# Kernel tuning notes

Hardware: AMD Instinct MI355X
Metric: run time of the kernel (lower is better)

Reference implementation:

```python
import jax, jax.numpy as jnp
import numpy as np

B, N, C = 8, 4096, 768
H, HD = 12, 64          # num_heads, head_dim = C // H
M = HD * 2              # rand_feat_dim
LAM = 0.3
NUM_STEP = 5


def setup_inputs() -> dict:
    key = jax.random.key(0)
    k1, k2, k3, k4 = jax.random.split(key, 4)
    x = jax.random.normal(k1, (B, N, C), dtype=jnp.float32)
    Wqkv = jax.random.normal(k2, (C, 2 * C), dtype=jnp.float32) * 0.02
    Wproj = jax.random.normal(k3, (C, C), dtype=jnp.float32) * 0.02
    bproj = jnp.zeros((C,), dtype=jnp.float32)
    rand_matrix = jax.random.normal(k4, (H, HD, M), dtype=jnp.float32)
    return {"x": x, "Wqkv": Wqkv, "Wproj": Wproj, "bproj": bproj,
            "rand_matrix": rand_matrix}


def _soft(z, t):
    # sign(z) * relu(|z| - t): soft-thresholding (ISTA proximal step)
    return jnp.sign(z) * jax.nn.relu(jnp.abs(z) - t)


def reference(x, Wqkv, Wproj, bproj, rand_matrix):
    Bn, Nn, Cn = x.shape
    Hh, hd, m = rand_matrix.shape
    scale = hd ** (-0.5)

    qkv = x @ Wqkv                                   # [B,N,2C]
    q = qkv[..., :Cn].reshape(Bn, Nn, Hh, hd).transpose(0, 2, 1, 3)  # [B,H,N,hd]
    v = qkv[..., Cn:].reshape(Bn, Nn, Hh, hd).transpose(0, 2, 1, 3)  # [B,H,N,hd]

    # random-feature map: exp(q @ proj - ||q||^2 / 2) / sqrt(m)
    qs = q * scale ** 0.5
    rf = jnp.exp(jnp.einsum('bhnd,hdm->bhnm', qs, rand_matrix)
                 - 0.5 * jnp.sum(qs * qs, axis=-1, keepdims=True)) / m ** 0.5
    # F.normalize(p=2, dim=-2): normalize over the sequence axis
    qn = rf / jnp.maximum(jnp.linalg.norm(rf, axis=-2, keepdims=True), 1e-12)

    kk = jnp.einsum('bhnm,bhnp->bhmp', qn, qn)       # [B,H,m,m]
    kv = jnp.einsum('bhnm,bhnd->bhmd', qn, v)        # [B,H,m,hd]

    # Lipschitz bound: max row L1 norm of kk, detached
    L = jax.lax.stop_gradient(
        jnp.max(jnp.sum(jnp.abs(kk), axis=-1), axis=-1))[..., None, None] + 1.0

    # unrolled ISTA soft-thresholding loop
    s = _soft(kv, LAM)
    for _ in range(NUM_STEP):
        s = _soft(s - (kk @ s - kv) / L, LAM / L)

    out = jnp.einsum('bhnm,bhmd->bhnd', qn, s)       # [B,H,N,hd]
    out = out.transpose(0, 2, 1, 3).reshape(Bn, Nn, Cn)
    return out @ Wproj + bproj
```

## Files before the change

kernel.cpp:

```cpp
#include <hip/hip_runtime.h>


typedef __attribute__((ext_vector_type(8))) short bf16x8;
typedef __attribute__((ext_vector_type(4))) float f32x4;

#define GLD16(gptr, lptr)                                                              \
  __builtin_amdgcn_global_load_lds((const __attribute__((address_space(1))) void*)(gptr), \
                                   (__attribute__((address_space(3))) void*)(lptr), 16, 0, 0)

__device__ __forceinline__ unsigned short f2bf(float f) {
  union { float f; unsigned int u; } v; v.f = f;
  unsigned int r = v.u + 0x7fffu + ((v.u >> 16) & 1u);
  return (unsigned short)(r >> 16);
}
__device__ __forceinline__ float bf2f(unsigned short s) {
  union { unsigned int u; float f; } v; v.u = ((unsigned int)s) << 16;
  return v.f;
}
__device__ __forceinline__ float rn_of(float css) {
  return 1.f / fmaxf(sqrtf(css), 1e-12f);
}

template<int NT>
__device__ __forceinline__ void gemm256_core(
    const unsigned short* __restrict__ A,
    const unsigned short* __restrict__ B,
    int ldk,
    f32x4 (&acc)[8][4],
    unsigned short* smem) {
  const int tid = threadIdx.x;
  const int lane = tid & 63, wave = tid >> 6;
  const int l16 = lane & 15, quad = lane >> 4;
  const int wr = wave >> 2, wc = wave & 3;
  const int rsw = l16 & 7;

#pragma unroll
  for (int i = 0; i < 8; i++)
#pragma unroll
    for (int j = 0; j < 4; j++)
#pragma unroll
      for (int r = 0; r < 4; r++) acc[i][j][r] = 0.f;

  const int srow0 = tid >> 3, sc0 = ((tid & 7) ^ (srow0 & 7)) << 3;
  const int srow1 = (tid + 512) >> 3, sc1 = ((tid & 7) ^ (srow1 & 7)) << 3;
  const int dstw = wave * 512;

  auto stage = [&](int T) {
    unsigned short* d0 = smem + (T & 1) * 32768;
#pragma unroll
    for (int h = 0; h < 2; h++) {
      const unsigned short* gA = A + (long)(h * 128) * ldk + T * 64;
      const unsigned short* gB = B + (long)(h * 128) * ldk + T * 64;
      GLD16(gA + (long)srow0 * ldk + sc0, d0 + h * 8192 + dstw);
      GLD16(gA + (long)srow1 * ldk + sc1, d0 + h * 8192 + 4096 + dstw);
      GLD16(gB + (long)srow0 * ldk + sc0, d0 + 16384 + h * 8192 + dstw);
      GLD16(gB + (long)srow1 * ldk + sc1, d0 + 16384 + h * 8192 + 4096 + dstw);
    }
  };

  bf16x8 afA[4], afB[4], bnA[4], bnB[4];

  auto rdA = [&](bf16x8 (&d)[4], int b, int mh, int ks) {
    const unsigned short* p = smem + b * 32768 + wr * 8192 + (mh * 64 + l16) * 64;
#pragma unroll
    for (int ii = 0; ii < 4; ii++)
      d[ii] = *(const bf16x8*)(p + ii * 1024 + (((ks * 4 + quad) ^ rsw) << 3));
  };
  auto rdB = [&](bf16x8 (&d)[4], int b, int ks) {
    const unsigned short* p = smem + b * 32768 + 16384 + (wc >> 1) * 8192 +
                              ((wc & 1) * 64 + l16) * 64;
#pragma unroll
    for (int jj = 0; jj < 4; jj++)
      d[jj] = *(const bf16x8*)(p + jj * 1024 + (((ks * 4 + quad) ^ rsw) << 3));
  };

  auto mma = [&](int mh, bf16x8 (&a)[4], bf16x8 (&bn)[4]) {
    __builtin_amdgcn_s_setprio(1);
#pragma unroll
    for (int ii = 0; ii < 4; ii++)
#pragma unroll
      for (int jj = 0; jj < 4; jj++)
        acc[mh * 4 + ii][jj] = __builtin_amdgcn_mfma_f32_16x16x32_bf16(
            a[ii], bn[jj], acc[mh * 4 + ii][jj], 0, 0, 0);
    __builtin_amdgcn_s_setprio(0);
  };

#define FENCE asm volatile("" ::: "memory")
#define SGB __builtin_amdgcn_sched_barrier(0)
#define LGKM(n) asm volatile("s_waitcnt lgkmcnt(" #n ")" ::: "memory")
#define VMC0 asm volatile("s_waitcnt vmcnt(0)" ::: "memory")

  stage(0); stage(1);
  asm volatile("s_waitcnt vmcnt(8)" ::: "memory");
  __builtin_amdgcn_s_barrier();
  rdA(afA, 0, 0, 0); rdB(bnA, 0, 0);
  FENCE;

#pragma unroll 1
  for (int t = 0; t < NT; t++) {
    const int b = t & 1;
    const bool last = (t == NT - 1);
    rdA(afB, b, 1, 0);
    LGKM(4); SGB;
    mma(0, afA, bnA);
    rdA(afA, b, 0, 1); rdB(bnB, b, 1);
    LGKM(8); SGB;
    mma(1, afB, bnA);
    VMC0; FENCE;
    __builtin_amdgcn_s_barrier();
    FENCE;
    rdA(afB, b, 1, 1);
    LGKM(4); SGB;
    mma(0, afA, bnB);
    if (!last) { rdA(afA, b ^ 1, 0, 0); rdB(bnA, b ^ 1, 0); LGKM(8); }
    else       { LGKM(0); }
    SGB;
    mma(1, afB, bnB);
    FENCE;
    __builtin_amdgcn_s_barrier();
    FENCE;
    if (t + 2 < NT) stage(t + 2);
  }
#undef FENCE
#undef SGB
#undef LGKM
#undef VMC0
}

__global__ __launch_bounds__(256) void k_convert_bf16(const float* __restrict__ in,
                                                      unsigned short* __restrict__ out, long n4) {
  long i = (long)blockIdx.x * 256 + threadIdx.x;
  if (i < n4) {
    float4 v = ((const float4*)in)[i];
    unsigned short o[4] = {f2bf(v.x), f2bf(v.y), f2bf(v.z), f2bf(v.w)};
    ((uint2*)out)[i] = *(uint2*)o;
  }
}

__global__ __launch_bounds__(256) void k_transpose_tiled(const float* __restrict__ in,
                                                         unsigned short* __restrict__ out,
                                                         int R, int C, float scale) {
  __shared__ float t[32][33];
  const float* ib = in + (long)blockIdx.z * R * C;
  unsigned short* ob = out + (long)blockIdx.z * R * C;
  int c0 = blockIdx.x * 32, r0 = blockIdx.y * 32;
  int tx = threadIdx.x & 31, ty = threadIdx.x >> 5;
#pragma unroll
  for (int k = 0; k < 32; k += 8)
    t[ty + k][tx] = ib[(long)(r0 + ty + k) * C + c0 + tx];
  __syncthreads();
#pragma unroll
  for (int k = 0; k < 32; k += 8)
    ob[(long)(c0 + ty + k) * R + r0 + tx] = f2bf(t[tx][ty + k] * scale);
}

__global__ __launch_bounds__(512, 2) void k_gemm_qkv256(const unsigned short* __restrict__ xbf,
                                                        const unsigned short* __restrict__ wqkvT,
                                                        unsigned short* __restrict__ q,
                                                        unsigned short* __restrict__ vT) {
  __shared__ __align__(16) unsigned short smem[65536];
  f32x4 acc[8][4];
  const int L = blockIdx.x;
  const int xcd = L & 7, slot = L >> 3;
  const int rt = xcd * 16 + slot / 6;
  const int ct = slot % 6;
  gemm256_core<12>(xbf + (long)rt * 256 * 768, wqkvT + (long)ct * 256 * 768, 768, acc, smem);

  const int tid = threadIdx.x, lane = tid & 63, wave = tid >> 6;
  const int l16 = lane & 15, quad = lane >> 4;
  const int wr = wave >> 2, wc = wave & 3;
  const int b = rt >> 4;
  const int nbase = (rt & 15) * 256;
  if (ct < 3) {
#pragma unroll
    for (int i = 0; i < 8; i++)
#pragma unroll
      for (int j = 0; j < 4; j++) {
        int col = ct * 256 + wc * 64 + j * 16 + l16;
        int h = col >> 6, d = col & 63;
#pragma unroll
        for (int r = 0; r < 4; r++) {
          int n = nbase + wr * 128 + i * 16 + quad * 4 + r;
          q[((long)(b * 12 + h) * 4096 + n) * 64 + d] = f2bf(acc[i][j][r]);
        }
      }
  } else {
    unsigned short* pool = smem;
    for (int hh = 0; hh < 2; hh++) {
      __syncthreads();
      if (wr == hh) {
#pragma unroll
        for (int i = 0; i < 8; i++)
#pragma unroll
          for (int j = 0; j < 4; j++)
#pragma unroll
            for (int r = 0; r < 4; r++)
              pool[(wc * 64 + j * 16 + l16) * 136 + i * 16 + quad * 4 + r] = f2bf(acc[i][j][r]);
      }
      __syncthreads();
#pragma unroll
      for (int it = 0; it < 8; it++) {
        int chunk = it * 512 + tid;
        int col = chunk >> 4, ng = chunk & 15;
        uint4 val = *(const uint4*)&pool[col * 136 + ng * 8];
        int vcol = (ct - 3) * 256 + col;
        int h = vcol >> 6, d = vcol & 63;
        long n = nbase + hh * 128 + ng * 8;
        *(uint4*)&vT[((long)(b * 12 + h) * 64 + d) * 4096 + n] = val;
      }
    }
  }
}

__global__ __launch_bounds__(256) void k_gemm_rf(const unsigned short* __restrict__ q,
                                                 const unsigned short* __restrict__ rmT,
                                                 unsigned short* __restrict__ qnT,
                                                 float* __restrict__ colss) {
  __shared__ __align__(16) unsigned short smem[16384];
  __shared__ float hnp[256];
  __shared__ float css[128];
  unsigned short* Asm = smem;
  unsigned short* Bsm = smem + 8192;
  unsigned short* pool = smem;
  f32x4 acc[4][4];
  const int nt = blockIdx.x, bh = blockIdx.y, h = bh % 12;
  const int tid = threadIdx.x, lane = tid & 63, wave = tid >> 6;
  const int l16 = lane & 15, quad = lane >> 4;
  const int wm = (wave >> 1) * 64, wn = (wave & 1) * 64;
  const int fsw = (l16 >> 1) & 3;
  const unsigned short* Aq = q + ((long)bh * 4096 + nt * 128) * 64;
  const unsigned short* Brm = rmT + (long)h * 8192;

#pragma unroll
  for (int c = 0; c < 4; c++) {
    int chunk = c * 256 + tid;
    int row = chunk >> 3, ko8 = chunk & 7;
    int kc = ko8 >> 2;
    int c2s = (ko8 & 3) ^ ((row >> 1) & 3);
    *(uint4*)(Asm + kc * 4096 + row * 32 + c2s * 8) = *(const uint4*)(Aq + (long)row * 64 + ko8 * 8);
    *(uint4*)(Bsm + kc * 4096 + row * 32 + c2s * 8) = *(const uint4*)(Brm + (long)row * 64 + ko8 * 8);
  }
  for (int i = tid; i < 128; i += 256) css[i] = 0.f;
  __syncthreads();
  {
    const unsigned short* ap = Asm + (tid & 1) * 4096 + (tid >> 1) * 32;
    float ssum = 0.f;
#pragma unroll
    for (int e = 0; e < 32; e++) { float f = bf2f(ap[e]); ssum += f * f; }
    hnp[tid] = ssum;
  }
#pragma unroll
  for (int i = 0; i < 4; i++)
#pragma unroll
    for (int j = 0; j < 4; j++)
#pragma unroll
      for (int r = 0; r < 4; r++) acc[i][j][r] = 0.f;
#pragma unroll
  for (int kc = 0; kc < 2; kc++) {
    bf16x8 af[4], bfr[4];
#pragma unroll
    for (int i = 0; i < 4; i++)
      af[i] = *(const bf16x8*)(Asm + kc * 4096 + (wm + i * 16 + l16) * 32 + ((quad ^ fsw) * 8));
#pragma unroll
    for (int j = 0; j < 4; j++)
      bfr[j] = *(const bf16x8*)(Bsm + kc * 4096 + (wn + j * 16 + l16) * 32 + ((quad ^ fsw) * 8));
#pragma unroll
    for (int i = 0; i < 4; i++)
#pragma unroll
      for (int j = 0; j < 4; j++)
        acc[i][j] = __builtin_amdgcn_mfma_f32_16x16x32_bf16(af[i], bfr[j], acc[i][j], 0, 0, 0);
  }
  __syncthreads();
  float hnv[4][4];
#pragma unroll
  for (int i = 0; i < 4; i++)
#pragma unroll
    for (int r = 0; r < 4; r++) {
      int row = wm + i * 16 + quad * 4 + r;
      hnv[i][r] = 0.0625f * (hnp[2 * row] + hnp[2 * row + 1]);
    }
#pragma unroll
  for (int j = 0; j < 4; j++) {
    int col = wn + j * 16 + l16;
    float cp = 0.f;
#pragma unroll
    for (int i = 0; i < 4; i++)
#pragma unroll
      for (int r = 0; r < 4; r++) {
        float v = __expf(acc[i][j][r] - hnv[i][r]) * 0.08838834764831845f;
        acc[i][j][r] = v;
        cp += v * v;
      }
    atomicAdd(&css[col], cp);
  }
  __syncthreads();
  for (int i = tid; i < 128; i += 256) atomicAdd(&colss[bh * 128 + i], css[i]);
  for (int hh = 0; hh < 2; hh++) {
    __syncthreads();
    if ((wave >> 1) == hh) {
#pragma unroll
      for (int i = 0; i < 4; i++)
#pragma unroll
        for (int j = 0; j < 4; j++)
#pragma unroll
          for (int r = 0; r < 4; r++)
            pool[(i * 16 + quad * 4 + r) * 134 + wn + j * 16 + l16] = f2bf(acc[i][j][r]);
    }
    __syncthreads();
#pragma unroll
    for (int c = 0; c < 4; c++) {
      int chunk = tid + c * 256;
      int m = chunk >> 3, nj = (chunk & 7) * 8;
      unsigned short o[8];
#pragma unroll
      for (int e = 0; e < 8; e++) o[e] = pool[(nj + e) * 134 + m];
      *(uint4*)&qnT[((long)bh * 128 + m) * 4096 + nt * 128 + hh * 64 + nj] = *(uint4*)o;
    }
  }
}

__global__ __launch_bounds__(256) void k_gemm_kkkv(const unsigned short* __restrict__ qnT,
                                                   const unsigned short* __restrict__ vT,
                                                   const float* __restrict__ colss,
                                                   unsigned short* __restrict__ kkp) {
  __shared__ __align__(16) unsigned short As[128 * 32], Bs[64 * 32];
  f32x4 acc[4][6];
  const int ks = blockIdx.x, bh = blockIdx.y;
  const unsigned short* A = qnT + (long)bh * 128 * 4096 + ks * 512;
  const unsigned short* B1 = vT + (long)bh * 64 * 4096 + ks * 512;
  const int tid = threadIdx.x, lane = tid & 63, wave = tid >> 6;
  const int l16 = lane & 15, quad = lane >> 4;
  const int wm = (wave >> 1) * 64, wn = (wave & 1) * 96;
  const int arow = tid >> 2;
  const int akos = (((tid & 3) ^ ((arow >> 1) & 3)) << 3);
  const int fsw = (l16 >> 1) & 3;
#pragma unroll
  for (int i = 0; i < 4; i++)
#pragma unroll
    for (int j = 0; j < 6; j++)
#pragma unroll
      for (int r = 0; r < 4; r++) acc[i][j][r] = 0.f;
  for (int k0 = 0; k0 < 512; k0 += 32) {
    __syncthreads();
    GLD16(A + (long)arow * 4096 + k0 + akos, As + wave * 512);
    GLD16(A + (long)(arow + 64) * 4096 + k0 + akos, As + 2048 + wave * 512);
    GLD16(B1 + (long)arow * 4096 + k0 + akos, Bs + wave * 512);
    __syncthreads();
    bf16x8 af[4], bfr[6];
#pragma unroll
    for (int i = 0; i < 4; i++)
      af[i] = *(const bf16x8*)(As + (wm + i * 16 + l16) * 32 + ((quad ^ fsw) * 8));
#pragma unroll
    for (int j = 0; j < 6; j++) {
      int row = wn + j * 16 + l16;
      const unsigned short* rp = (row < 128) ? (As + row * 32) : (Bs + (row - 128) * 32);
      bfr[j] = *(const bf16x8*)(rp + ((quad ^ fsw) * 8));
    }
#pragma unroll
    for (int i = 0; i < 4; i++)
#pragma unroll
      for (int j = 0; j < 6; j++)
        acc[i][j] = __builtin_amdgcn_mfma_f32_16x16x32_bf16(af[i], bfr[j], acc[i][j], 0, 0, 0);
  }
  unsigned short* dst = kkp + ((long)ks * 96 + bh) * 24576;
  float rnr[4][4];
#pragma unroll
  for (int i = 0; i < 4; i++)
#pragma unroll
    for (int r = 0; r < 4; r++)
      rnr[i][r] = rn_of(colss[bh * 128 + wm + i * 16 + quad * 4 + r]);
#pragma unroll
  for (int j = 0; j < 6; j++) {
    int col = wn + j * 16 + l16;
    float rnc = (col < 128) ? rn_of(colss[bh * 128 + col]) : 1.f;
#pragma unroll
    for (int i = 0; i < 4; i++)
#pragma unroll
      for (int r = 0; r < 4; r++) {
        int row = wm + i * 16 + quad * 4 + r;
        dst[row * 192 + col] = f2bf(acc[i][j][r] * rnr[i][r] * rnc);
      }
  }
}

__global__ __launch_bounds__(256) void k_ista(const unsigned short* __restrict__ kkp,
                                              const float* __restrict__ colss,
                                              unsigned short* __restrict__ sT) {
  __shared__ __align__(16) unsigned short kks[128 * 144];
  __shared__ __align__(16) unsigned short ssT[64 * 144];
  __shared__ float kvs[128 * 64];
  __shared__ float red[128];
  __shared__ float rns[128];
  const int tid = threadIdx.x, lane = tid & 63, wave = tid >> 6;
  const int l16 = lane & 15, quad = lane >> 4;
  const int wm = (wave >> 1) * 64, wn = (wave & 1) * 32;
  const int bh = blockIdx.x;
  const unsigned short* base = kkp + (long)bh * 24576;
  for (int idx = tid; idx < 3072; idx += 256) {
    int m = idx / 24, c8 = idx % 24;
    float f[8] = {0.f, 0.f, 0.f, 0.f, 0.f, 0.f, 0.f, 0.f};
#pragma unroll
    for (int ks = 0; ks < 8; ks++) {
      union { uint4 u; unsigned short s[8]; } u;
      u.u = *(const uint4*)(base + (long)ks * 2359296 + m * 192 + c8 * 8);
#pragma unroll
      for (int e = 0; e < 8; e++) f[e] += bf2f(u.s[e]);
    }
    if (c8 < 16) {
#pragma unroll
      for (int e = 0; e < 8; e++) kks[m * 144 + c8 * 8 + e] = f2bf(f[e]);
    } else {
#pragma unroll
      for (int e = 0; e < 8; e++) kvs[m * 64 + (c8 - 16) * 8 + e] = f[e];
    }
  }
  __syncthreads();
  float kv[4][2][4];
#pragma unroll
  for (int i = 0; i < 4; i++)
#pragma unroll
    for (int j = 0; j < 2; j++)
#pragma unroll
      for (int r = 0; r < 4; r++) {
        int m = wm + i * 16 + quad * 4 + r, d = wn + j * 16 + l16;
        kv[i][j][r] = kvs[m * 64 + d];
      }
  if (tid < 128) {
    float rs = 0.f;
    const unsigned short* rp = kks + tid * 144;
    for (int p = 0; p < 128; p++) rs += fabsf(bf2f(rp[p]));
    red[tid] = rs;
    rns[tid] = rn_of(colss[bh * 128 + tid]);
  }
  __syncthreads();
  for (int o = 64; o > 0; o >>= 1) {
    if (tid < o) red[tid] = fmaxf(red[tid], red[tid + o]);
    __syncthreads();
  }
  const float L = red[0] + 1.f;
  const float invL = 1.f / L;
  const float lamL = 0.3f * invL;
  float sreg[4][2][4];
#pragma unroll
  for (int i = 0; i < 4; i++)
#pragma unroll
    for (int j = 0; j < 2; j++)
#pragma unroll
      for (int r = 0; r < 4; r++) {
        float z = kv[i][j][r];
        float az = fabsf(z) - 0.3f;
        float s = az > 0.f ? copysignf(az, z) : 0.f;
        sreg[i][j][r] = s;
        ssT[(wn + j * 16 + l16) * 144 + wm + i * 16 + quad * 4 + r] = f2bf(s);
      }
  for (int step = 0; step < 5; step++) {
    __syncthreads();
    f32x4 acc[4][2];
#pragma unroll
    for (int i = 0; i < 4; i++)
#pragma unroll
      for (int j = 0; j < 2; j++)
#pragma unroll
        for (int r = 0; r < 4; r++) acc[i][j][r] = 0.f;
#pragma unroll
    for (int kc = 0; kc < 4; kc++) {
      bf16x8 af[4], bfj[2];
#pragma unroll
      for (int i = 0; i < 4; i++)
        af[i] = *(const bf16x8*)(kks + (wm + i * 16 + l16) * 144 + kc * 32 + quad * 8);
#pragma unroll
      for (int j = 0; j < 2; j++)
        bfj[j] = *(const bf16x8*)(ssT + (wn + j * 16 + l16) * 144 + kc * 32 + quad * 8);
#pragma unroll
      for (int i = 0; i < 4; i++)
#pragma unroll
        for (int j = 0; j < 2; j++)
          acc[i][j] = __builtin_amdgcn_mfma_f32_16x16x32_bf16(af[i], bfj[j], acc[i][j], 0, 0, 0);
    }
    __syncthreads();
#pragma unroll
    for (int i = 0; i < 4; i++)
#pragma unroll
      for (int j = 0; j < 2; j++)
#pragma unroll
        for (int r = 0; r < 4; r++) {
          float z = sreg[i][j][r] - (acc[i][j][r] - kv[i][j][r]) * invL;
          float az = fabsf(z) - lamL;
          float s = az > 0.f ? copysignf(az, z) : 0.f;
          sreg[i][j][r] = s;
          ssT[(wn + j * 16 + l16) * 144 + wm + i * 16 + quad * 4 + r] = f2bf(s);
        }
  }
#pragma unroll
  for (int i = 0; i < 4; i++)
#pragma unroll
    for (int j = 0; j < 2; j++)
#pragma unroll
      for (int r = 0; r < 4; r++) {
        int m = wm + i * 16 + quad * 4 + r, d = wn + j * 16 + l16;
        sT[(long)bh * 8192 + d * 128 + m] = f2bf(sreg[i][j][r] * rns[m]);
      }
}

__global__ __launch_bounds__(256) void k_gemm_attn(const unsigned short* __restrict__ qnT,
                                                   const unsigned short* __restrict__ sT,
                                                   unsigned short* __restrict__ attn) {
  __shared__ __align__(16) unsigned short As2[4352];
  __shared__ __align__(16) unsigned short Bs[64 * 32];
  f32x4 acc[4][2];
  const int nt = blockIdx.x, bh = blockIdx.y;
  const int b = bh / 12, h = bh % 12;
  const int tid = threadIdx.x, lane = tid & 63, wave = tid >> 6;
  const int l16 = lane & 15, quad = lane >> 4;
  const int wm = (wave >> 1) * 64, wn = (wave & 1) * 32;
  const int fsw = (l16 >> 1) & 3;
#pragma unroll
  for (int i = 0; i < 4; i++)
#pragma unroll
    for (int j = 0; j < 2; j++)
#pragma unroll
      for (int r = 0; r < 4; r++) acc[i][j][r] = 0.f;
  for (int k0 = 0; k0 < 128; k0 += 32) {
    __syncthreads();
#pragma unroll
    for (int it = 0; it < 3; it++) {
      if (it < 2 || tid < 32) {
        int c = it * 256 + tid;
        int p = (c * 241) >> 12;
        int nh = c - p * 17;
        int k = ((p & 7) << 2) + (p >> 3);
        int n8 = (nh < 16 ? nh : 15) << 3;
        const unsigned short* gp = qnT + ((long)bh * 128 + k0 + k) * 4096 + nt * 128 + n8;
        GLD16(gp, As2 + (it * 256 + wave * 64) * 8);
      }
    }
    {
      int dd = tid >> 2;
      int ko = (((tid & 3) ^ ((dd >> 1) & 3)) * 8);
      const unsigned short* gp = sT + ((long)bh * 64 + dd) * 128 + k0 + ko;
      GLD16(gp, Bs + wave * 512);
    }
    __syncthreads();
    bf16x8 af[4], bfr[2];
#pragma unroll
    for (int i = 0; i < 4; i++) {
      union { bf16x8 v; unsigned short s[8]; } u;
#pragma unroll
      for (int e = 0; e < 8; e++) {
        int p = ((e & 3) << 3) + (quad << 1) + (e >> 2);
        u.s[e] = As2[p * 136 + wm + i * 16 + l16];
      }
      af[i] = u.v;
    }
#pragma unroll
    for (int j = 0; j < 2; j++)
      bfr[j] = *(const bf16x8*)&Bs[(wn + j * 16 + l16) * 32 + ((quad ^ fsw) * 8)];
#pragma unroll
    for (int i = 0; i < 4; i++)
#pragma unroll
      for (int j = 0; j < 2; j++)
        acc[i][j] = __builtin_amdgcn_mfma_f32_16x16x32_bf16(af[i], bfr[j], acc[i][j], 0, 0, 0);
  }
#pragma unroll
  for (int i = 0; i < 4; i++)
#pragma unroll
    for (int j = 0; j < 2; j++)
#pragma unroll
      for (int r = 0; r < 4; r++) {
        int n = nt * 128 + wm + i * 16 + quad * 4 + r;
        int dd = wn + j * 16 + l16;
        attn[((long)b * 4096 + n) * 768 + h * 64 + dd] = f2bf(acc[i][j][r]);
      }
}

__global__ __launch_bounds__(512, 2) void k_gemm_proj256(const unsigned short* __restrict__ attn,
                                                         const unsigned short* __restrict__ wprojT,
                                                         const float* __restrict__ bias,
                                                         float* __restrict__ out) {
  __shared__ __align__(16) unsigned short smem[65536];
  f32x4 acc[8][4];
  const int L = blockIdx.x;
  const int xcd = L & 7, slot = L >> 3;
  const int rt = xcd * 16 + slot / 3;
  const int ct = slot % 3;
  gemm256_core<12>(attn + (long)rt * 256 * 768, wprojT + (long)ct * 256 * 768, 768, acc, smem);
  const int tid = threadIdx.x, lane = tid & 63, wave = tid >> 6;
  const int l16 = lane & 15, quad = lane >> 4;
  const int wr = wave >> 2, wc = wave & 3;
  const long row0 = (long)rt * 256 + wr * 128;
#pragma unroll
  for (int i = 0; i < 8; i++)
#pragma unroll
    for (int j = 0; j < 4; j++) {
      int col = ct * 256 + wc * 64 + j * 16 + l16;
      float bv = bias[col];
#pragma unroll
      for (int r = 0; r < 4; r++) {
        long row = row0 + i * 16 + quad * 4 + r;
        out[row * 768 + col] = acc[i][j][r] + bv;
      }
    }
}

extern "C" void kernel_launch(void* const* d_in, const int* in_sizes, int n_in,
                              void* d_out, int out_size, void* d_ws, size_t ws_size,
                              hipStream_t stream) {
  const float* x = (const float*)d_in[0];
  const float* Wqkv = (const float*)d_in[1];
  const float* Wproj = (const float*)d_in[2];
  const float* bproj = (const float*)d_in[3];
  const float* rm = (const float*)d_in[4];
  float* out = (float*)d_out;

  size_t o = 0;
  char* wsb = (char*)d_ws;
  auto take = [&](size_t b) { char* p = wsb + o; o += b; return p; };
  unsigned short* wqkvT = (unsigned short*)take(2359296);
  unsigned short* wprojT = (unsigned short*)take(1179648);
  unsigned short* rmT = (unsigned short*)take(196608);
  unsigned short* q = (unsigned short*)take(50331648);
  unsigned short* vT = (unsigned short*)take(50331648);
  float* colss = (float*)take(49152);
  unsigned short* sT = (unsigned short*)take(1572864);
  if (ws_size < o) return;

  unsigned short* xbf = (unsigned short*)d_out;
  unsigned short* qnT = (unsigned short*)d_out;
  unsigned short* kkp = q;
  unsigned short* attnbf = q;

  hipMemsetAsync(colss, 0, 49152, stream);

  k_convert_bf16<<<24576, 256, 0, stream>>>(x, xbf, 6291456L);
  k_transpose_tiled<<<dim3(48, 24, 1), 256, 0, stream>>>(Wqkv, wqkvT, 768, 1536, 1.0f);
  k_transpose_tiled<<<dim3(24, 24, 1), 256, 0, stream>>>(Wproj, wprojT, 768, 768, 1.0f);
  k_transpose_tiled<<<dim3(4, 2, 12), 256, 0, stream>>>(rm, rmT, 64, 128, 0.3535533905932738f);
  k_gemm_qkv256<<<768, 512, 0, stream>>>(xbf, wqkvT, q, vT);
  k_gemm_rf<<<dim3(32, 96), 256, 0, stream>>>(q, rmT, qnT, colss);
  k_gemm_kkkv<<<dim3(8, 96), 256, 0, stream>>>(qnT, vT, colss, kkp);
  k_ista<<<96, 256, 0, stream>>>(kkp, colss, sT);
  k_gemm_attn<<<dim3(32, 96), 256, 0, stream>>>(qnT, sT, attnbf);
  k_gemm_proj256<<<384, 512, 0, stream>>>(attnbf, wprojT, bproj, out);
}
```

Measured before the change: 455.4 us.

## Shrink QKV/proj GEMM tiles to 128x256 with BK=32 and split ISTA reduction

The 256x256, BK=64 GEMM core with its deep software-pipelined fragment prefetch is replaced by a simpler 128x256, BK=32 core with smaller LDS use and four blocks per CU. Both the QKV and projection GEMMs now launch twice as many blocks. Separately, the split-K reduction of the kk/kv partials moves out of the 96-block ISTA kernel into a new, wider reduction kernel, and ISTA now just loads the reduced results. The aim is more parallelism and occupancy, at the cost of less operand reuse per tile, a less overlapped inner loop, and one extra kernel launch.

```diff
diff --git a/kernel.cpp b/kernel.cpp
--- a/kernel.cpp
+++ b/kernel.cpp
@@ -22,109 +22,77 @@
 }
 
 template<int NT>
-__device__ __forceinline__ void gemm256_core(
+__device__ __forceinline__ void gemm_bk32_core(
     const unsigned short* __restrict__ A,
     const unsigned short* __restrict__ B,
     int ldk,
-    f32x4 (&acc)[8][4],
+    f32x4 (&acc)[4][4],
     unsigned short* smem) {
   const int tid = threadIdx.x;
   const int lane = tid & 63, wave = tid >> 6;
   const int l16 = lane & 15, quad = lane >> 4;
   const int wr = wave >> 2, wc = wave & 3;
-  const int rsw = l16 & 7;
-
-#pragma unroll
-  for (int i = 0; i < 8; i++)
-#pragma unroll
-    for (int j = 0; j < 4; j++)
-#pragma unroll
-      for (int r = 0; r < 4; r++) acc[i][j][r] = 0.f;
-
-  const int srow0 = tid >> 3, sc0 = ((tid & 7) ^ (srow0 & 7)) << 3;
-  const int srow1 = (tid + 512) >> 3, sc1 = ((tid & 7) ^ (srow1 & 7)) << 3;
+  const int fsw = (l16 >> 1) & 3;
+
+#pragma unroll
+  for (int m = 0; m < 4; m++)
+#pragma unroll
+    for (int n = 0; n < 4; n++)
+#pragma unroll
+      for (int r = 0; r < 4; r++) acc[m][n][r] = 0.f;
+
+  const int arow = tid >> 2;
+  const int asw = (((tid & 3) ^ ((arow >> 1) & 3)) << 3);
   const int dstw = wave * 512;
 
   auto stage = [&](int T) {
-    unsigned short* d0 = smem + (T & 1) * 32768;
-#pragma unroll
-    for (int h = 0; h < 2; h++) {
-      const unsigned short* gA = A + (long)(h * 128) * ldk + T * 64;
-      const unsigned short* gB = B + (long)(h * 128) * ldk + T * 64;
-      GLD16(gA + (long)srow0 * ldk + sc0, d0 + h * 8192 + dstw);
-      GLD16(gA + (long)srow1 * ldk + sc1, d0 + h * 8192 + 4096 + dstw);
-      GLD16(gB + (long)srow0 * ldk + sc0, d0 + 16384 + h * 8192 + dstw);
-      GLD16(gB + (long)srow1 * ldk + sc1, d0 + 16384 + h * 8192 + 4096 + dstw);
-    }
+    unsigned short* d = smem + (T & 1) * 12288;
+    GLD16(A + (long)arow * ldk + T * 32 + asw, d + dstw);
+    GLD16(B + (long)arow * ldk + T * 32 + asw, d + 4096 + dstw);
+    GLD16(B + (long)(arow + 128) * ldk + T * 32 + asw, d + 8192 + dstw);
   };
 
-  bf16x8 afA[4], afB[4], bnA[4], bnB[4];
-
-  auto rdA = [&](bf16x8 (&d)[4], int b, int mh, int ks) {
-    const unsigned short* p = smem + b * 32768 + wr * 8192 + (mh * 64 + l16) * 64;
-#pragma unroll
-    for (int ii = 0; ii < 4; ii++)
-      d[ii] = *(const bf16x8*)(p + ii * 1024 + (((ks * 4 + quad) ^ rsw) << 3));
-  };
-  auto rdB = [&](bf16x8 (&d)[4], int b, int ks) {
-    const unsigned short* p = smem + b * 32768 + 16384 + (wc >> 1) * 8192 +
-                              ((wc & 1) * 64 + l16) * 64;
-#pragma unroll
-    for (int jj = 0; jj < 4; jj++)
-      d[jj] = *(const bf16x8*)(p + jj * 1024 + (((ks * 4 + quad) ^ rsw) << 3));
-  };
-
-  auto mma = [&](int mh, bf16x8 (&a)[4], bf16x8 (&bn)[4]) {
-    __builtin_amdgcn_s_setprio(1);
-#pragma unroll
-    for (int ii = 0; ii < 4; ii++)
-#pragma unroll
-      for (int jj = 0; jj < 4; jj++)
-        acc[mh * 4 + ii][jj] = __builtin_amdgcn_mfma_f32_16x16x32_bf16(
-            a[ii], bn[jj], acc[mh * 4 + ii][jj], 0, 0, 0);
-    __builtin_amdgcn_s_setprio(0);
+  bf16x8 af[4], bn[4];
+  auto rdAB = [&](int b) {
+    const unsigned short* Ab = smem + b * 12288;
+    const unsigned short* Bb = Ab + 4096;
+#pragma unroll
+    for (int m = 0; m < 4; m++)
+      af[m] = *(const bf16x8*)(Ab + (wr * 64 + m * 16 + l16) * 32 + ((quad ^ fsw) << 3));
+#pragma unroll
+    for (int n = 0; n < 4; n++)
+      bn[n] = *(const bf16x8*)(Bb + (wc * 64 + n * 16 + l16) * 32 + ((quad ^ fsw) << 3));
   };
 
 #define FENCE asm volatile("" ::: "memory")
 #define SGB __builtin_amdgcn_sched_barrier(0)
-#define LGKM(n) asm volatile("s_waitcnt lgkmcnt(" #n ")" ::: "memory")
-#define VMC0 asm volatile("s_waitcnt vmcnt(0)" ::: "memory")
 
   stage(0); stage(1);
-  asm volatile("s_waitcnt vmcnt(8)" ::: "memory");
+  asm volatile("s_waitcnt vmcnt(3)" ::: "memory");
   __builtin_amdgcn_s_barrier();
-  rdA(afA, 0, 0, 0); rdB(bnA, 0, 0);
-  FENCE;
 
 #pragma unroll 1
   for (int t = 0; t < NT; t++) {
     const int b = t & 1;
-    const bool last = (t == NT - 1);
-    rdA(afB, b, 1, 0);
-    LGKM(4); SGB;
-    mma(0, afA, bnA);
-    rdA(afA, b, 0, 1); rdB(bnB, b, 1);
-    LGKM(8); SGB;
-    mma(1, afB, bnA);
-    VMC0; FENCE;
-    __builtin_amdgcn_s_barrier();
-    FENCE;
-    rdA(afB, b, 1, 1);
-    LGKM(4); SGB;
-    mma(0, afA, bnB);
-    if (!last) { rdA(afA, b ^ 1, 0, 0); rdB(bnA, b ^ 1, 0); LGKM(8); }
-    else       { LGKM(0); }
-    SGB;
-    mma(1, afB, bnB);
-    FENCE;
-    __builtin_amdgcn_s_barrier();
-    FENCE;
+    rdAB(b);
+    asm volatile("s_waitcnt lgkmcnt(0)" ::: "memory"); SGB;
+    __builtin_amdgcn_s_setprio(1);
+#pragma unroll
+    for (int m = 0; m < 4; m++)
+#pragma unroll
+      for (int n = 0; n < 4; n++)
+        acc[m][n] = __builtin_amdgcn_mfma_f32_16x16x32_bf16(af[m], bn[n], acc[m][n], 0, 0, 0);
+    __builtin_amdgcn_s_setprio(0);
+    FENCE; __builtin_amdgcn_s_barrier();
     if (t + 2 < NT) stage(t + 2);
+    if (t + 1 < NT) {
+      if (t + 2 < NT) { asm volatile("s_waitcnt vmcnt(3)" ::: "memory"); }
+      else            { asm volatile("s_waitcnt vmcnt(0)" ::: "memory"); }
+      FENCE; __builtin_amdgcn_s_barrier();
+    }
   }
 #undef FENCE
 #undef SGB
-#undef LGKM
-#undef VMC0
 }
 
 __global__ __launch_bounds__(256) void k_convert_bf16(const float* __restrict__ in,
@@ -154,34 +122,34 @@
     ob[(long)(c0 + ty + k) * R + r0 + tx] = f2bf(t[tx][ty + k] * scale);
 }
 
-__global__ __launch_bounds__(512, 2) void k_gemm_qkv256(const unsigned short* __restrict__ xbf,
+__global__ __launch_bounds__(512, 4) void k_gemm_qkv128(const unsigned short* __restrict__ xbf,
                                                         const unsigned short* __restrict__ wqkvT,
                                                         unsigned short* __restrict__ q,
                                                         unsigned short* __restrict__ vT) {
-  __shared__ __align__(16) unsigned short smem[65536];
-  f32x4 acc[8][4];
+  __shared__ __align__(16) unsigned short smem[24576];
+  f32x4 acc[4][4];
   const int L = blockIdx.x;
   const int xcd = L & 7, slot = L >> 3;
-  const int rt = xcd * 16 + slot / 6;
+  const int rt = xcd * 32 + slot / 6;
   const int ct = slot % 6;
-  gemm256_core<12>(xbf + (long)rt * 256 * 768, wqkvT + (long)ct * 256 * 768, 768, acc, smem);
+  gemm_bk32_core<24>(xbf + (long)rt * 128 * 768, wqkvT + (long)ct * 256 * 768, 768, acc, smem);
 
   const int tid = threadIdx.x, lane = tid & 63, wave = tid >> 6;
   const int l16 = lane & 15, quad = lane >> 4;
   const int wr = wave >> 2, wc = wave & 3;
-  const int b = rt >> 4;
-  const int nbase = (rt & 15) * 256;
+  const int b = rt >> 5;
+  const int nbase = (rt & 31) * 128;
   if (ct < 3) {
 #pragma unroll
-    for (int i = 0; i < 8; i++)
-#pragma unroll
-      for (int j = 0; j < 4; j++) {
-        int col = ct * 256 + wc * 64 + j * 16 + l16;
+    for (int m = 0; m < 4; m++)
+#pragma unroll
+      for (int n = 0; n < 4; n++) {
+        int col = ct * 256 + wc * 64 + n * 16 + l16;
         int h = col >> 6, d = col & 63;
 #pragma unroll
         for (int r = 0; r < 4; r++) {
-          int n = nbase + wr * 128 + i * 16 + quad * 4 + r;
-          q[((long)(b * 12 + h) * 4096 + n) * 64 + d] = f2bf(acc[i][j][r]);
+          int nr = nbase + wr * 64 + m * 16 + quad * 4 + r;
+          q[((long)(b * 12 + h) * 4096 + nr) * 64 + d] = f2bf(acc[m][n][r]);
         }
       }
   } else {
@@ -190,22 +158,22 @@
       __syncthreads();
       if (wr == hh) {
 #pragma unroll
-        for (int i = 0; i < 8; i++)
-#pragma unroll
-          for (int j = 0; j < 4; j++)
+        for (int m = 0; m < 4; m++)
+#pragma unroll
+          for (int n = 0; n < 4; n++)
 #pragma unroll
             for (int r = 0; r < 4; r++)
-              pool[(wc * 64 + j * 16 + l16) * 136 + i * 16 + quad * 4 + r] = f2bf(acc[i][j][r]);
+              pool[(wc * 64 + n * 16 + l16) * 72 + m * 16 + quad * 4 + r] = f2bf(acc[m][n][r]);
       }
       __syncthreads();
 #pragma unroll
-      for (int it = 0; it < 8; it++) {
-        int chunk = it * 512 + tid;
-        int col = chunk >> 4, ng = chunk & 15;
-        uint4 val = *(const uint4*)&pool[col * 136 + ng * 8];
+      for (int c = 0; c < 4; c++) {
+        int chunk = c * 512 + tid;
+        int col = chunk >> 3, ng = chunk & 7;
+        uint4 val = *(const uint4*)&pool[col * 72 + ng * 8];
         int vcol = (ct - 3) * 256 + col;
         int h = vcol >> 6, d = vcol & 63;
-        long n = nbase + hh * 128 + ng * 8;
+        long n = nbase + hh * 64 + ng * 8;
         *(uint4*)&vT[((long)(b * 12 + h) * 64 + d) * 4096 + n] = val;
       }
     }
@@ -383,9 +351,41 @@
   }
 }
 
-__global__ __launch_bounds__(256) void k_ista(const unsigned short* __restrict__ kkp,
-                                              const float* __restrict__ colss,
-                                              unsigned short* __restrict__ sT) {
+__global__ __launch_bounds__(256) void k_red(const unsigned short* __restrict__ kkp,
+                                             unsigned short* __restrict__ kkred,
+                                             float* __restrict__ kvred) {
+  const int g = blockIdx.x, bh = blockIdx.y;
+  const int tid = threadIdx.x;
+  const unsigned short* base = kkp + (long)bh * 24576 + (long)(g * 32) * 192;
+#pragma unroll
+  for (int c = 0; c < 3; c++) {
+    int idx = c * 256 + tid;
+    int m = idx / 24, c8 = idx % 24;
+    float f[8] = {0.f, 0.f, 0.f, 0.f, 0.f, 0.f, 0.f, 0.f};
+#pragma unroll
+    for (int ks = 0; ks < 8; ks++) {
+      union { uint4 u; unsigned short s[8]; } u;
+      u.u = *(const uint4*)(base + (long)ks * 2359296 + m * 192 + c8 * 8);
+#pragma unroll
+      for (int e = 0; e < 8; e++) f[e] += bf2f(u.s[e]);
+    }
+    long row = (long)bh * 128 + g * 32 + m;
+    if (c8 < 16) {
+      unsigned short o[8];
+#pragma unroll
+      for (int e = 0; e < 8; e++) o[e] = f2bf(f[e]);
+      *(uint4*)&kkred[row * 128 + c8 * 8] = *(uint4*)o;
+    } else {
+      *(float4*)&kvred[row * 64 + (c8 - 16) * 8] = make_float4(f[0], f[1], f[2], f[3]);
+      *(float4*)&kvred[row * 64 + (c8 - 16) * 8 + 4] = make_float4(f[4], f[5], f[6], f[7]);
+    }
+  }
+}
+
+__global__ __launch_bounds__(256) void k_ista2(const unsigned short* __restrict__ kkred,
+                                               const float* __restrict__ kvred,
+                                               const float* __restrict__ colss,
+                                               unsigned short* __restrict__ sT) {
   __shared__ __align__(16) unsigned short kks[128 * 144];
   __shared__ __align__(16) unsigned short ssT[64 * 144];
   __shared__ float kvs[128 * 64];
@@ -395,24 +395,15 @@
   const int l16 = lane & 15, quad = lane >> 4;
   const int wm = (wave >> 1) * 64, wn = (wave & 1) * 32;
   const int bh = blockIdx.x;
-  const unsigned short* base = kkp + (long)bh * 24576;
-  for (int idx = tid; idx < 3072; idx += 256) {
-    int m = idx / 24, c8 = idx % 24;
-    float f[8] = {0.f, 0.f, 0.f, 0.f, 0.f, 0.f, 0.f, 0.f};
-#pragma unroll
-    for (int ks = 0; ks < 8; ks++) {
-      union { uint4 u; unsigned short s[8]; } u;
-      u.u = *(const uint4*)(base + (long)ks * 2359296 + m * 192 + c8 * 8);
-#pragma unroll
-      for (int e = 0; e < 8; e++) f[e] += bf2f(u.s[e]);
-    }
-    if (c8 < 16) {
-#pragma unroll
-      for (int e = 0; e < 8; e++) kks[m * 144 + c8 * 8 + e] = f2bf(f[e]);
-    } else {
-#pragma unroll
-      for (int e = 0; e < 8; e++) kvs[m * 64 + (c8 - 16) * 8 + e] = f[e];
-    }
+  for (int idx = tid; idx < 2048; idx += 256) {
+    int m = idx >> 4, c8 = idx & 15;
+    uint4 v = *(const uint4*)(kkred + ((long)bh * 128 + m) * 128 + c8 * 8);
+    *(uint4*)&kks[m * 144 + c8 * 8] = v;
+  }
+  for (int idx = tid; idx < 2048; idx += 256) {
+    int m = idx >> 4, c4 = idx & 15;
+    float4 v = *(const float4*)(kvred + ((long)bh * 128 + m) * 64 + c4 * 4);
+    *(float4*)&kvs[m * 64 + c4 * 4] = v;
   }
   __syncthreads();
   float kv[4][2][4];
@@ -573,31 +564,31 @@
       }
 }
 
-__global__ __launch_bounds__(512, 2) void k_gemm_proj256(const unsigned short* __restrict__ attn,
+__global__ __launch_bounds__(512, 4) void k_gemm_proj128(const unsigned short* __restrict__ attn,
                                                          const unsigned short* __restrict__ wprojT,
                                                          const float* __restrict__ bias,
                                                          float* __restrict__ out) {
-  __shared__ __align__(16) unsigned short smem[65536];
-  f32x4 acc[8][4];
+  __shared__ __align__(16) unsigned short smem[24576];
+  f32x4 acc[4][4];
   const int L = blockIdx.x;
   const int xcd = L & 7, slot = L >> 3;
-  const int rt = xcd * 16 + slot / 3;
+  const int rt = xcd * 32 + slot / 3;
   const int ct = slot % 3;
-  gemm256_core<12>(attn + (long)rt * 256 * 768, wprojT + (long)ct * 256 * 768, 768, acc, smem);
+  gemm_bk32_core<24>(attn + (long)rt * 128 * 768, wprojT + (long)ct * 256 * 768, 768, acc, smem);
   const int tid = threadIdx.x, lane = tid & 63, wave = tid >> 6;
   const int l16 = lane & 15, quad = lane >> 4;
   const int wr = wave >> 2, wc = wave & 3;
-  const long row0 = (long)rt * 256 + wr * 128;
-#pragma unroll
-  for (int i = 0; i < 8; i++)
-#pragma unroll
-    for (int j = 0; j < 4; j++) {
-      int col = ct * 256 + wc * 64 + j * 16 + l16;
+  const long row0 = (long)rt * 128 + wr * 64;
+#pragma unroll
+  for (int m = 0; m < 4; m++)
+#pragma unroll
+    for (int n = 0; n < 4; n++) {
+      int col = ct * 256 + wc * 64 + n * 16 + l16;
       float bv = bias[col];
 #pragma unroll
       for (int r = 0; r < 4; r++) {
-        long row = row0 + i * 16 + quad * 4 + r;
-        out[row * 768 + col] = acc[i][j][r] + bv;
+        long row = row0 + m * 16 + quad * 4 + r;
+        out[row * 768 + col] = acc[m][n][r] + bv;
       }
     }
 }
@@ -628,6 +619,8 @@
   unsigned short* qnT = (unsigned short*)d_out;
   unsigned short* kkp = q;
   unsigned short* attnbf = q;
+  unsigned short* kkred = vT;
+  float* kvred = (float*)(vT + 1572864);
 
   hipMemsetAsync(colss, 0, 49152, stream);
 
@@ -635,10 +628,11 @@
   k_transpose_tiled<<<dim3(48, 24, 1), 256, 0, stream>>>(Wqkv, wqkvT, 768, 1536, 1.0f);
   k_transpose_tiled<<<dim3(24, 24, 1), 256, 0, stream>>>(Wproj, wprojT, 768, 768, 1.0f);
   k_transpose_tiled<<<dim3(4, 2, 12), 256, 0, stream>>>(rm, rmT, 64, 128, 0.3535533905932738f);
-  k_gemm_qkv256<<<768, 512, 0, stream>>>(xbf, wqkvT, q, vT);
+  k_gemm_qkv128<<<1536, 512, 0, stream>>>(xbf, wqkvT, q, vT);
   k_gemm_rf<<<dim3(32, 96), 256, 0, stream>>>(q, rmT, qnT, colss);
   k_gemm_kkkv<<<dim3(8, 96), 256, 0, stream>>>(qnT, vT, colss, kkp);
-  k_ista<<<96, 256, 0, stream>>>(kkp, colss, sT);
+  k_red<<<dim3(4, 96), 256, 0, stream>>>(kkp, kkred, kvred);
+  k_ista2<<<96, 256, 0, stream>>>(kkred, kvred, colss, sT);
   k_gemm_attn<<<dim3(32, 96), 256, 0, stream>>>(qnT, sT, attnbf);
-  k_gemm_proj256<<<384, 512, 0, stream>>>(attnbf, wprojT, bproj, out);
-}
+  k_gemm_proj128<<<768, 512, 0, stream>>>(attnbf, wprojT, bproj, out);
+}
```

Measured after the change: 459.1 us. No clear change (+0.8%).
